# Kernel optimization log

Hardware: AMD Instinct MI355X
Metric: run time of the kernel (lower is better)

## Reference

```python
import jax, jax.numpy as jnp
import numpy as np

NINP = 1024
NHID = 1024
STEPS = 8
INITRANGE = 0.04
T, B = 256, 64

# DARTS_V1 recurrent genotype: (activation, predecessor-state index)
GENOTYPE = [("sigmoid", 0), ("relu", 1), ("relu", 1), ("identity", 1),
            ("tanh", 2), ("sigmoid", 5), ("tanh", 3), ("relu", 5)]

ACT = {
    "tanh": jnp.tanh,
    "relu": jax.nn.relu,
    "sigmoid": jax.nn.sigmoid,
    "identity": lambda x: x,
    "selu": jax.nn.selu,
}


def setup_inputs() -> dict:
    key = jax.random.key(0)
    k_in, k_w0, k_ws = jax.random.split(key, 3)
    inputs = jax.random.normal(k_in, (T, B, NINP), dtype=jnp.float32)
    hidden = jnp.zeros((1, B, NHID), dtype=jnp.float32)
    W0 = jax.random.uniform(k_w0, (NINP + NHID, 2 * NHID),
                            minval=-INITRANGE, maxval=INITRANGE, dtype=jnp.float32)
    Ws = jax.random.uniform(k_ws, (STEPS, NHID, 2 * NHID),
                            minval=-INITRANGE, maxval=INITRANGE, dtype=jnp.float32)
    return {"inputs": inputs, "hidden": hidden, "W0": W0, "Ws": Ws}


def _cell(x, h_prev, W0, Ws):
    # init state: highway combine of gated candidate with previous hidden
    xh = jnp.concatenate([x, h_prev], axis=-1)            # [B, ninp+nhid]
    c0, h0 = jnp.split(xh @ W0, 2, axis=-1)               # [B, nhid] each
    s0 = h_prev + jax.nn.sigmoid(c0) * (jnp.tanh(h0) - h_prev)
    states = [s0]
    for i, (name, pred) in enumerate(GENOTYPE):
        s_prev = states[pred]
        c, h = jnp.split(s_prev @ Ws[i], 2, axis=-1)      # [B, nhid] each
        s = s_prev + jax.nn.sigmoid(c) * (ACT[name](h) - s_prev)
        states.append(s)
    # output = mean over the DAG intermediate states (concat = range(1, steps+1))
    return jnp.mean(jnp.stack(states[1:], axis=0), axis=0)


def reference(inputs, hidden, W0, Ws):
    h0 = hidden[0]                                        # [B, nhid]

    def step(h, x_t):
        h_new = _cell(x_t, h, W0, Ws)
        return h_new, h_new

    _, hiddens = jax.lax.scan(step, h0, inputs)           # [T, B, nhid]
    return hiddens
```

## Files before the change

kernel.cpp:

```cpp
#include <hip/hip_runtime.h>
#include <math.h>


typedef __attribute__((ext_vector_type(8))) _Float16 half8;
typedef __attribute__((ext_vector_type(4))) float f32x4;
typedef __attribute__((ext_vector_type(4))) unsigned int u32x4;
typedef __attribute__((ext_vector_type(8))) unsigned short us8;

#define NH 1024
#define SCALE 2048.f
#define INVS  (1.f/2048.f)
#define WF_BYTES 83886080ull
#define FA_BYTES 1572864ull
#define T_STEPS  256

#define WBAR() asm volatile("s_barrier" ::: "memory")
#define LBAR() asm volatile("s_waitcnt lgkmcnt(0)\n\ts_barrier" ::: "memory")

__device__ __forceinline__ float sigf(float x){ return 1.f/(1.f+__expf(-x)); }
__device__ __forceinline__ void limbs2(float x, _Float16& a, _Float16& b){
    a = (_Float16)x; b = (_Float16)((x - (float)a)*SCALE);
}

struct Pre { const float* W0; const float* Ws; unsigned short* wf; };

__global__ __launch_bounds__(256) void preconv(Pre d) {
    int gid  = blockIdx.x * 4 + (threadIdx.x >> 6);
    int lane = threadIdx.x & 63;
    const float* W; unsigned short* dst; int nks, cg, ks;
    if (gid < 8192) {
        W = d.W0; dst = d.wf; nks = 64; cg = gid >> 6; ks = gid & 63;
    } else {
        int g = gid - 8192; int mm = g >> 12; int wi = g & 4095;
        W   = d.Ws + (size_t)mm * (1024 * 2048);
        dst = d.wf + 8388608ull + (size_t)mm * 4194304ull;
        nks = 32; cg = wi >> 5; ks = wi & 31;
    }
    int c  = cg * 16 + (lane & 15);
    int kb = ks * 32 + (lane >> 4) * 8;
    half8 h0, h1;
    #pragma unroll
    for (int j = 0; j < 8; ++j) {
        _Float16 p, q; limbs2(W[(size_t)(kb + j) * 2048 + c], p, q);
        h0[j] = p; h1[j] = q;
    }
    unsigned short* o = dst + ((size_t)cg * nks + ks) * 1024 + lane * 8;
    *(half8*)o         = h0;
    *(half8*)(o + 512) = h1;
}

__global__ __launch_bounds__(256) void initk(const float* hidden, char* fa, unsigned* flags) {
    int gid = blockIdx.x * 256 + threadIdx.x;
    if (gid < 1536) flags[gid] = (gid < 256) ? 1u : 0u;
    #pragma unroll
    for (int e = 0; e < 4; ++e) {
        int i = gid * 4 + e;
        int row = i >> 10, col = i & 1023;
        int rt = row >> 4, rowf = row & 15;
        int ksp = col >> 5, kin = col & 31;
        int lanep = (kin >> 3) * 16 + rowf;
        size_t off = (size_t)rt * 65536 + ((size_t)ksp * 64 + lanep) * 32 + (kin & 7) * 4;
        _Float16 u0, u1; limbs2(hidden[i], u0, u1);
        unsigned pk = (unsigned)__builtin_bit_cast(unsigned short, u0) |
                      ((unsigned)__builtin_bit_cast(unsigned short, u1) << 16);
        *(unsigned*)(fa + off) = pk;
    }
}

__device__ __forceinline__ void aload(const char* fa, int ks, int lane, half8& a0, half8& a1) {
    const char* p = fa + ((size_t)ks * 64 + lane) * 32;
    us8 q0 = *(const us8*)p;
    us8 q1 = *(const us8*)(p + 16);
    a0 = __builtin_bit_cast(half8, __builtin_shufflevector(q0, q1, 0,2,4,6,8,10,12,14));
    a1 = __builtin_bit_cast(half8, __builtin_shufflevector(q0, q1, 1,3,5,7,9,11,13,15));
}
__device__ __forceinline__ half8 ldw(const unsigned short* p) { return *(const half8*)p; }
__device__ __forceinline__ void mfma6(half8 a0, half8 a1, half8 w0, half8 w1,
                                      f32x4& x0, f32x4& x1) {
    x0 = __builtin_amdgcn_mfma_f32_16x16x32_f16(a0, w0, x0, 0, 0, 0);
    x1 = __builtin_amdgcn_mfma_f32_16x16x32_f16(a0, w1, x1, 0, 0, 0);
    x1 = __builtin_amdgcn_mfma_f32_16x16x32_f16(a1, w0, x1, 0, 0, 0);
}
__device__ __forceinline__ void rwrite1(float* arena, int wave, int lane,
        f32x4 c0, f32x4 c1, f32x4 h0, f32x4 h1) {
    float* b = arena + wave * 512;
    #pragma unroll
    for (int r = 0; r < 4; ++r) {
        b[lane * 4 + r]       = c0[r] + c1[r] * INVS;
        b[256 + lane * 4 + r] = h0[r] + h1[r] * INVS;
    }
}
__device__ __forceinline__ void rsum1(const float* arena, int idx, float& cs, float& hs) {
    float c = 0.f, h = 0.f;
    #pragma unroll
    for (int w = 0; w < 8; ++w) {
        c += arena[w * 512 + idx];
        h += arena[w * 512 + 256 + idx];
    }
    cs = c; hs = h;
}
__device__ __forceinline__ void fstore(char* fa, int offp, float v) {
    _Float16 u0, u1; limbs2(v, u0, u1);
    unsigned pk = (unsigned)__builtin_bit_cast(unsigned short, u0) |
                  ((unsigned)__builtin_bit_cast(unsigned short, u1) << 16);
    __hip_atomic_store((unsigned*)(fa + offp), pk, __ATOMIC_RELAXED, __HIP_MEMORY_SCOPE_AGENT);
}
template<int ACQ>
__device__ __forceinline__ void pollw(unsigned* f, unsigned tgt, int lane) {
    unsigned v = __hip_atomic_load(f + lane, __ATOMIC_RELAXED, __HIP_MEMORY_SCOPE_AGENT);
    while (__ballot(v < tgt)) {
        __builtin_amdgcn_s_sleep(2);
        v = __hip_atomic_load(f + lane, __ATOMIC_RELAXED, __HIP_MEMORY_SCOPE_AGENT);
    }
    if (ACQ)
        (void)__hip_atomic_load(f, __ATOMIC_ACQUIRE, __HIP_MEMORY_SCOPE_AGENT);
}
__device__ __forceinline__ void publish(unsigned* slot, unsigned v) {
    __hip_atomic_store(slot, v, __ATOMIC_RELAXED, __HIP_MEMORY_SCOPE_AGENT);
}

struct PK {
    const float* x; const float* hidden;
    const unsigned short* wf;
    char* fa; unsigned* flags; float* out;
};

__global__ __launch_bounds__(512, 2) void persist(PK p) {
    __shared__ unsigned short slab[65536];
    __shared__ float arena[4096];

    const int tid  = threadIdx.x;
    const int wave = tid >> 6, lane = tid & 63;
    const int l15 = lane & 15, lg = lane >> 4;
    const int lane8 = lane * 8, lg8 = lg * 8;
    const int bx = blockIdx.x;
    const int cg = (bx & 7) * 8 + ((bx >> 3) & 7);
    const int rt = bx >> 6;

    const unsigned short* wf0 = p.wf;
    const unsigned short* wfs[8];
    #pragma unroll
    for (int i = 0; i < 8; ++i) wfs[i] = p.wf + 8388608ull + (size_t)i * 4194304ull;

    char* FAH  = p.fa + (size_t)(0 * 4 + rt) * 65536;
    char* FAS0 = p.fa + (size_t)(1 * 4 + rt) * 65536;
    char* FAS1 = p.fa + (size_t)(2 * 4 + rt) * 65536;
    char* FAS2 = p.fa + (size_t)(3 * 4 + rt) * 65536;
    char* FAS3 = p.fa + (size_t)(4 * 4 + rt) * 65536;
    char* FAS5 = p.fa + (size_t)(5 * 4 + rt) * 65536;
    #define FLG(tn) (p.flags + ((tn) * 4 + rt) * 64)

    #define PFW(dst, wfp) do { \
        _Pragma("unroll") \
        for (int _i = 0; _i < 4; ++_i) { \
            const int _ks = wave * 4 + _i; \
            const unsigned short* _pc = (wfp) + ((size_t)cg * 32 + _ks) * 1024 + lane8; \
            const unsigned short* _ph = (wfp) + ((size_t)(cg + 64) * 32 + _ks) * 1024 + lane8; \
            dst[_i*4+0] = ldw(_pc); dst[_i*4+1] = ldw(_pc + 512); \
            dst[_i*4+2] = ldw(_ph); dst[_i*4+3] = ldw(_ph + 512); } } while (0)
    #define PFWX(dst) do { \
        _Pragma("unroll") \
        for (int _i = 0; _i < 4; ++_i) { \
            const int _ks = wave * 4 + _i; \
            const unsigned short* _pc = wf0 + ((size_t)cg * 64 + _ks) * 1024 + lane8; \
            const unsigned short* _ph = wf0 + ((size_t)(cg + 64) * 64 + _ks) * 1024 + lane8; \
            dst[_i*4+0] = ldw(_pc); dst[_i*4+1] = ldw(_pc + 512); \
            dst[_i*4+2] = ldw(_ph); dst[_i*4+3] = ldw(_ph + 512); } } while (0)
    #define ALD(dst0, dst1, fa) do { \
        _Pragma("unroll") \
        for (int _i = 0; _i < 4; ++_i) aload(fa, wave * 4 + _i, lane, dst0[_i], dst1[_i]); } while (0)
    #define MFM(w, a0v, a1v, X0, X1, Y0, Y1) do { \
        _Pragma("unroll") \
        for (int _i = 0; _i < 4; ++_i) { \
            mfma6(a0v[_i], a1v[_i], w[_i*4+0], w[_i*4+1], X0, X1); \
            mfma6(a0v[_i], a1v[_i], w[_i*4+2], w[_i*4+3], Y0, Y1); } } while (0)

    {
        const u32x4* sc = (const u32x4*)(wf0 + ((size_t)cg * 64 + 32) * 1024);
        const u32x4* sh = (const u32x4*)(wf0 + ((size_t)(cg + 64) * 64 + 32) * 1024);
        u32x4* dst = (u32x4*)slab;
        for (int i = tid; i < 4096; i += 512) { dst[i] = sc[i]; dst[4096 + i] = sh[i]; }
    }

    const int rowf = tid >> 4, colf = tid & 15;
    const size_t opos = (size_t)(rt * 16 + rowf) * NH + cg * 16 + colf;
    const int idx = colf * 4 + (rowf >> 2) * 64 + (rowf & 3);
    int offp;
    {
        int col = cg * 16 + colf;
        int ksp = col >> 5, kin = col & 31;
        int lanep = (kin >> 3) * 16 + rowf;
        offp = (ksp * 64 + lanep) * 32 + (kin & 7) * 4;
    }
    float hprev = 0.f, s0v = 0.f, s1v = 0.f, s2v = 0.f, s3v = 0.f, s5v = 0.f, runsum = 0.f;
    if (tid < 256) hprev = p.hidden[opos];
    const int xrow = rt * 16 + l15;
    __syncthreads();

    half8 wA[16], wB[16];
    PFW(wA, wfs[0]);
    PFWX(wB);

    for (int t = 0; t < T_STEPS; ++t) {
        const float* xt = p.x + (size_t)t * 65536;

        f32x4 c0 = {}, c1 = {}, h0 = {}, h1 = {};
        {
            half8 xa0[4], xa1[4];
            #pragma unroll
            for (int i = 0; i < 4; ++i) {
                const int ks = wave * 4 + i;
                const float* xp = xt + (size_t)xrow * NH + ks * 32 + lg8;
                float4 v0 = *(const float4*)xp, v1 = *(const float4*)(xp + 4);
                float fv[8] = {v0.x, v0.y, v0.z, v0.w, v1.x, v1.y, v1.z, v1.w};
                #pragma unroll
                for (int j = 0; j < 8; ++j) { _Float16 u, w2; limbs2(fv[j], u, w2); xa0[i][j] = u; xa1[i][j] = w2; }
            }
            if (wave == 7) {
                pollw<1>(FLG(0), t + 1, lane);
                asm volatile("s_waitcnt vmcnt(0)" ::: "memory");
            }
            MFM(wB, xa0, xa1, c0, c1, h0, h1);
        }
        WBAR();
        {
            half8 ha0[4], ha1[4];
            ALD(ha0, ha1, FAH);
            #pragma unroll
            for (int i = 0; i < 4; ++i) {
                const int kc = wave * 4 + i;
                const unsigned short* pc = &slab[kc * 1024 + lane8];
                const unsigned short* ph = &slab[(kc + 32) * 1024 + lane8];
                mfma6(ha0[i], ha1[i], *(const half8*)pc, *(const half8*)(pc + 512), c0, c1);
                mfma6(ha0[i], ha1[i], *(const half8*)ph, *(const half8*)(ph + 512), h0, h1);
            }
            rwrite1(arena, wave, lane, c0, c1, h0, h1);
        }
        LBAR();
        if (tid < 256) {
            float cs, hs; rsum1(arena, idx, cs, hs);
            s0v = hprev + sigf(cs) * (tanhf(hs) - hprev);
            fstore(FAS0, offp, s0v);
        }
        __syncthreads();
        if (tid == 0) publish(FLG(1) + cg, t + 1);
        PFW(wB, wfs[1]);

        if (wave == 7) pollw<0>(FLG(1), t + 1, lane);
        WBAR();
        half8 a0[4], a1[4];
        {
            ALD(a0, a1, FAS0);
            f32x4 X0 = {}, X1 = {}, Y0 = {}, Y1 = {};
            MFM(wA, a0, a1, X0, X1, Y0, Y1);
            rwrite1(arena, wave, lane, X0, X1, Y0, Y1);
        }
        LBAR();
        if (tid < 256) {
            float cs, hs; rsum1(arena, idx, cs, hs);
            s1v = s0v + sigf(cs) * (sigf(hs) - s0v);
            fstore(FAS1, offp, s1v);
            runsum = s1v;
        }
        __syncthreads();
        if (tid == 0) publish(FLG(2) + cg, t + 1);
        PFW(wA, wfs[2]);

        if (wave == 7) pollw<0>(FLG(2), t + 1, lane);
        WBAR();
        ALD(a0, a1, FAS1);
        {
            f32x4 X0 = {}, X1 = {}, Y0 = {}, Y1 = {};
            MFM(wB, a0, a1, X0, X1, Y0, Y1);
            rwrite1(arena, wave, lane, X0, X1, Y0, Y1);
        }
        LBAR();
        if (tid < 256) {
            float cs, hs; rsum1(arena, idx, cs, hs);
            s2v = s1v + sigf(cs) * (fmaxf(hs, 0.f) - s1v);
            fstore(FAS2, offp, s2v);
        }
        __syncthreads();
        if (tid == 0) publish(FLG(3) + cg, t + 1);
        PFW(wB, wfs[3]);
        {
            f32x4 X0 = {}, X1 = {}, Y0 = {}, Y1 = {};
            MFM(wA, a0, a1, X0, X1, Y0, Y1);
            rwrite1(arena, wave, lane, X0, X1, Y0, Y1);
        }
        LBAR();
        if (tid < 256) {
            float cs, hs; rsum1(arena, idx, cs, hs);
            s3v = s1v + sigf(cs) * (fmaxf(hs, 0.f) - s1v);
            fstore(FAS3, offp, s3v);
        }
        __syncthreads();
        if (tid == 0) publish(FLG(4) + cg, t + 1);
        PFW(wA, wfs[4]);
        {
            f32x4 X0 = {}, X1 = {}, Y0 = {}, Y1 = {};
            MFM(wB, a0, a1, X0, X1, Y0, Y1);
            rwrite1(arena, wave, lane, X0, X1, Y0, Y1);
        }
        LBAR();
        if (tid < 256) {
            float cs, hs; rsum1(arena, idx, cs, hs);
            float s4v = s1v + sigf(cs) * (hs - s1v);
            runsum += s2v + s3v + s4v;
        }
        WBAR();
        PFW(wB, wfs[6]);

        if (wave == 7) { pollw<0>(FLG(3), t + 1, lane); pollw<0>(FLG(4), t + 1, lane); }
        WBAR();
        {
            half8 b0[4], b1[4];
            ALD(a0, a1, FAS2);
            ALD(b0, b1, FAS3);
            f32x4 X0 = {}, X1 = {}, Y0 = {}, Y1 = {};
            MFM(wA, a0, a1, X0, X1, Y0, Y1);
            f32x4 U0 = {}, U1 = {}, V0 = {}, V1 = {};
            MFM(wB, b0, b1, U0, U1, V0, V1);
            rwrite1(arena, wave, lane, X0, X1, Y0, Y1);
            LBAR();
            if (tid < 256) {
                float cs, hs; rsum1(arena, idx, cs, hs);
                s5v = s2v + sigf(cs) * (tanhf(hs) - s2v);
                fstore(FAS5, offp, s5v);
            }
            __syncthreads();
            if (tid == 0) publish(FLG(5) + cg, t + 1);
            PFW(wA, wfs[5]);
            rwrite1(arena, wave, lane, U0, U1, V0, V1);
            LBAR();
            if (tid < 256) {
                float cs, hs; rsum1(arena, idx, cs, hs);
                float s7v = s3v + sigf(cs) * (tanhf(hs) - s3v);
                runsum += s5v + s7v;
            }
            WBAR();
            PFW(wB, wfs[7]);
        }

        if (wave == 7) pollw<0>(FLG(5), t + 1, lane);
        WBAR();
        {
            ALD(a0, a1, FAS5);
            f32x4 X0 = {}, X1 = {}, Y0 = {}, Y1 = {};
            MFM(wA, a0, a1, X0, X1, Y0, Y1);
            f32x4 U0 = {}, U1 = {}, V0 = {}, V1 = {};
            MFM(wB, a0, a1, U0, U1, V0, V1);
            rwrite1(arena, wave, lane, X0, X1, Y0, Y1);
            LBAR();
            float c6 = 0.f, h6 = 0.f;
            if (tid < 256) rsum1(arena, idx, c6, h6);
            LBAR();
            PFW(wA, wfs[0]);
            rwrite1(arena, wave, lane, U0, U1, V0, V1);
            LBAR();
            if (tid < 256) {
                float c8, h8; rsum1(arena, idx, c8, h8);
                float s6 = s5v + sigf(c6) * (sigf(h6) - s5v);
                float s8 = s5v + sigf(c8) * (fmaxf(h8, 0.f) - s5v);
                float v = 0.125f * (runsum + s6 + s8);
                p.out[(size_t)t * 65536 + opos] = v;
                fstore(FAH, offp, v);
                hprev = v;
            }
            __syncthreads();
            if (tid == 0) publish(FLG(0) + cg, t + 2);
            PFWX(wB);
        }
    }
    #undef FLG
    #undef PFW
    #undef PFWX
    #undef ALD
    #undef MFM
}

extern "C" void kernel_launch(void* const* d_in, const int* in_sizes, int n_in,
                              void* d_out, int out_size, void* d_ws, size_t ws_size,
                              hipStream_t stream) {
    (void)in_sizes; (void)n_in; (void)out_size; (void)ws_size;
    const float* inputs = (const float*)d_in[0];
    const float* hidden = (const float*)d_in[1];
    const float* W0     = (const float*)d_in[2];
    const float* Ws     = (const float*)d_in[3];
    float* out = (float*)d_out;

    char* base = (char*)d_ws;
    unsigned short* wf = (unsigned short*)base;
    char* fa = base + WF_BYTES;
    unsigned* flags = (unsigned*)(fa + FA_BYTES);

    initk<<<64, 256, 0, stream>>>(hidden, fa, flags);
    preconv<<<10240, 256, 0, stream>>>(Pre{W0, Ws, wf});

    PK pk{inputs, hidden, wf, fa, flags, out};
    void* args[] = {&pk};
    if (hipLaunchCooperativeKernel((void*)persist, dim3(256), dim3(512), args, 0, stream) != hipSuccess)
        persist<<<256, 512, 0, stream>>>(pk);
}
```

Baseline: 9.756 ms.

## Stream weights via global_load_lds into a double-buffered LDS ring

Replaces the register-held weight prefetch (two 16-entry half8 buffers) and the static LDS slab holding the hidden part of W0 with a two-slot LDS ring. Each slot is filled by direct global-to-LDS loads, and the next weight block is issued right after the current one is consumed. The aim is to free VGPRs and let the load engine overlap weight fetches with MFMA work. In exchange, prefetch depth drops to one half-matrix ahead. The recurrent W0 slice is now re-streamed from global memory every step. Correctness relies on the barriers draining the async LDS loads, since only lgkmcnt waits are added explicitly.

```diff
diff --git a/kernel.cpp b/kernel.cpp
--- a/kernel.cpp
+++ b/kernel.cpp
@@ -4,7 +4,6 @@
 
 typedef __attribute__((ext_vector_type(8))) _Float16 half8;
 typedef __attribute__((ext_vector_type(4))) float f32x4;
-typedef __attribute__((ext_vector_type(4))) unsigned int u32x4;
 typedef __attribute__((ext_vector_type(8))) unsigned short us8;
 
 #define NH 1024
@@ -14,8 +13,11 @@
 #define FA_BYTES 1572864ull
 #define T_STEPS  256
 
-#define WBAR() asm volatile("s_barrier" ::: "memory")
-#define LBAR() asm volatile("s_waitcnt lgkmcnt(0)\n\ts_barrier" ::: "memory")
+#define LGKM0() asm volatile("s_waitcnt lgkmcnt(0)" ::: "memory")
+#define LBAR()  asm volatile("s_waitcnt lgkmcnt(0)\n\ts_barrier" ::: "memory")
+
+typedef const __attribute__((address_space(1))) void* gas_ptr;
+typedef __attribute__((address_space(3))) void* las_ptr;
 
 __device__ __forceinline__ float sigf(float x){ return 1.f/(1.f+__expf(-x)); }
 __device__ __forceinline__ void limbs2(float x, _Float16& a, _Float16& b){
@@ -74,7 +76,6 @@
     a0 = __builtin_bit_cast(half8, __builtin_shufflevector(q0, q1, 0,2,4,6,8,10,12,14));
     a1 = __builtin_bit_cast(half8, __builtin_shufflevector(q0, q1, 1,3,5,7,9,11,13,15));
 }
-__device__ __forceinline__ half8 ldw(const unsigned short* p) { return *(const half8*)p; }
 __device__ __forceinline__ void mfma6(half8 a0, half8 a1, half8 w0, half8 w1,
                                       f32x4& x0, f32x4& x1) {
     x0 = __builtin_amdgcn_mfma_f32_16x16x32_f16(a0, w0, x0, 0, 0, 0);
@@ -126,21 +127,32 @@
 };
 
 __global__ __launch_bounds__(512, 2) void persist(PK p) {
-    __shared__ unsigned short slab[65536];
+    __shared__ char ring[2][65536];
     __shared__ float arena[4096];
 
-    const int tid  = threadIdx.x;
+    const int tid = threadIdx.x;
     const int wave = tid >> 6, lane = tid & 63;
     const int l15 = lane & 15, lg = lane >> 4;
-    const int lane8 = lane * 8, lg8 = lg * 8;
+    const int lg8 = lg * 8;
     const int bx = blockIdx.x;
     const int cg = (bx & 7) * 8 + ((bx >> 3) & 7);
     const int rt = bx >> 6;
 
     const unsigned short* wf0 = p.wf;
-    const unsigned short* wfs[8];
-    #pragma unroll
-    for (int i = 0; i < 8; ++i) wfs[i] = p.wf + 8388608ull + (size_t)i * 4194304ull;
+    const unsigned short* gB[20];
+    {
+        gB[0] = wf0 + (size_t)(cg * 64) * 1024;
+        gB[1] = wf0 + (size_t)((cg + 64) * 64) * 1024;
+        gB[2] = wf0 + (size_t)(cg * 64 + 32) * 1024;
+        gB[3] = wf0 + (size_t)((cg + 64) * 64 + 32) * 1024;
+        const int mo[8] = {0, 1, 2, 3, 4, 6, 5, 7};
+        #pragma unroll
+        for (int u = 0; u < 8; ++u) {
+            const unsigned short* wm = p.wf + 8388608ull + (size_t)mo[u] * 4194304ull;
+            gB[4 + 2 * u]     = wm + (size_t)cg * 32768;
+            gB[4 + 2 * u + 1] = wm + (size_t)(cg + 64) * 32768;
+        }
+    }
 
     char* FAH  = p.fa + (size_t)(0 * 4 + rt) * 65536;
     char* FAS0 = p.fa + (size_t)(1 * 4 + rt) * 65536;
@@ -150,37 +162,27 @@
     char* FAS5 = p.fa + (size_t)(5 * 4 + rt) * 65536;
     #define FLG(tn) (p.flags + ((tn) * 4 + rt) * 64)
 
-    #define PFW(dst, wfp) do { \
+    #define DMA(b) do { \
+        const char* _g = (const char*)gB[b] + wave * 8192 + lane * 16; \
+        char* _l = &ring[(b) & 1][wave * 8192]; \
+        _Pragma("unroll") \
+        for (int _i = 0; _i < 8; ++_i) \
+            __builtin_amdgcn_global_load_lds((gas_ptr)(_g + _i * 1024), \
+                                             (las_ptr)(_l + _i * 1024), 16, 0, 0); \
+    } while (0)
+    #define CONS(b, A0, A1, X0, X1) do { \
         _Pragma("unroll") \
         for (int _i = 0; _i < 4; ++_i) { \
-            const int _ks = wave * 4 + _i; \
-            const unsigned short* _pc = (wfp) + ((size_t)cg * 32 + _ks) * 1024 + lane8; \
-            const unsigned short* _ph = (wfp) + ((size_t)(cg + 64) * 32 + _ks) * 1024 + lane8; \
-            dst[_i*4+0] = ldw(_pc); dst[_i*4+1] = ldw(_pc + 512); \
-            dst[_i*4+2] = ldw(_ph); dst[_i*4+3] = ldw(_ph + 512); } } while (0)
-    #define PFWX(dst) do { \
-        _Pragma("unroll") \
-        for (int _i = 0; _i < 4; ++_i) { \
-            const int _ks = wave * 4 + _i; \
-            const unsigned short* _pc = wf0 + ((size_t)cg * 64 + _ks) * 1024 + lane8; \
-            const unsigned short* _ph = wf0 + ((size_t)(cg + 64) * 64 + _ks) * 1024 + lane8; \
-            dst[_i*4+0] = ldw(_pc); dst[_i*4+1] = ldw(_pc + 512); \
-            dst[_i*4+2] = ldw(_ph); dst[_i*4+3] = ldw(_ph + 512); } } while (0)
+            const char* _p = &ring[(b) & 1][(wave * 4 + _i) * 2048 + lane * 16]; \
+            half8 _w0 = *(const half8*)_p; \
+            half8 _w1 = *(const half8*)(_p + 1024); \
+            mfma6(A0[_i], A1[_i], _w0, _w1, X0, X1); \
+        } \
+    } while (0)
     #define ALD(dst0, dst1, fa) do { \
         _Pragma("unroll") \
-        for (int _i = 0; _i < 4; ++_i) aload(fa, wave * 4 + _i, lane, dst0[_i], dst1[_i]); } while (0)
-    #define MFM(w, a0v, a1v, X0, X1, Y0, Y1) do { \
-        _Pragma("unroll") \
-        for (int _i = 0; _i < 4; ++_i) { \
-            mfma6(a0v[_i], a1v[_i], w[_i*4+0], w[_i*4+1], X0, X1); \
-            mfma6(a0v[_i], a1v[_i], w[_i*4+2], w[_i*4+3], Y0, Y1); } } while (0)
-
-    {
-        const u32x4* sc = (const u32x4*)(wf0 + ((size_t)cg * 64 + 32) * 1024);
-        const u32x4* sh = (const u32x4*)(wf0 + ((size_t)(cg + 64) * 64 + 32) * 1024);
-        u32x4* dst = (u32x4*)slab;
-        for (int i = tid; i < 4096; i += 512) { dst[i] = sc[i]; dst[4096 + i] = sh[i]; }
-    }
+        for (int _i = 0; _i < 4; ++_i) aload(fa, wave * 4 + _i, lane, dst0[_i], dst1[_i]); \
+    } while (0)
 
     const int rowf = tid >> 4, colf = tid & 15;
     const size_t opos = (size_t)(rt * 16 + rowf) * NH + cg * 16 + colf;
@@ -195,14 +197,13 @@
     float hprev = 0.f, s0v = 0.f, s1v = 0.f, s2v = 0.f, s3v = 0.f, s5v = 0.f, runsum = 0.f;
     if (tid < 256) hprev = p.hidden[opos];
     const int xrow = rt * 16 + l15;
+
+    DMA(0); DMA(1);
     __syncthreads();
-
-    half8 wA[16], wB[16];
-    PFW(wA, wfs[0]);
-    PFWX(wB);
 
     for (int t = 0; t < T_STEPS; ++t) {
         const float* xt = p.x + (size_t)t * 65536;
+        half8 a0[4], a1[4];
 
         f32x4 c0 = {}, c1 = {}, h0 = {}, h1 = {};
         {
@@ -216,24 +217,16 @@
                 #pragma unroll
                 for (int j = 0; j < 8; ++j) { _Float16 u, w2; limbs2(fv[j], u, w2); xa0[i][j] = u; xa1[i][j] = w2; }
             }
-            if (wave == 7) {
-                pollw<1>(FLG(0), t + 1, lane);
-                asm volatile("s_waitcnt vmcnt(0)" ::: "memory");
-            }
-            MFM(wB, xa0, xa1, c0, c1, h0, h1);
-        }
-        WBAR();
+            CONS(0, xa0, xa1, c0, c1); LGKM0(); DMA(2);
+            CONS(1, xa0, xa1, h0, h1); LGKM0(); DMA(3);
+        }
+        if (wave == 7) pollw<1>(FLG(0), t + 1, lane);
+        __syncthreads();
         {
             half8 ha0[4], ha1[4];
             ALD(ha0, ha1, FAH);
-            #pragma unroll
-            for (int i = 0; i < 4; ++i) {
-                const int kc = wave * 4 + i;
-                const unsigned short* pc = &slab[kc * 1024 + lane8];
-                const unsigned short* ph = &slab[(kc + 32) * 1024 + lane8];
-                mfma6(ha0[i], ha1[i], *(const half8*)pc, *(const half8*)(pc + 512), c0, c1);
-                mfma6(ha0[i], ha1[i], *(const half8*)ph, *(const half8*)(ph + 512), h0, h1);
-            }
+            CONS(2, ha0, ha1, c0, c1); LGKM0(); DMA(4);
+            CONS(3, ha0, ha1, h0, h1); LGKM0(); DMA(5);
             rwrite1(arena, wave, lane, c0, c1, h0, h1);
         }
         LBAR();
@@ -244,15 +237,14 @@
         }
         __syncthreads();
         if (tid == 0) publish(FLG(1) + cg, t + 1);
-        PFW(wB, wfs[1]);
 
         if (wave == 7) pollw<0>(FLG(1), t + 1, lane);
-        WBAR();
-        half8 a0[4], a1[4];
-        {
-            ALD(a0, a1, FAS0);
-            f32x4 X0 = {}, X1 = {}, Y0 = {}, Y1 = {};
-            MFM(wA, a0, a1, X0, X1, Y0, Y1);
+        __syncthreads();
+        ALD(a0, a1, FAS0);
+        {
+            f32x4 X0 = {}, X1 = {}, Y0 = {}, Y1 = {};
+            CONS(4, a0, a1, X0, X1); LGKM0(); DMA(6);
+            CONS(5, a0, a1, Y0, Y1); LGKM0(); DMA(7);
             rwrite1(arena, wave, lane, X0, X1, Y0, Y1);
         }
         LBAR();
@@ -264,14 +256,14 @@
         }
         __syncthreads();
         if (tid == 0) publish(FLG(2) + cg, t + 1);
-        PFW(wA, wfs[2]);
 
         if (wave == 7) pollw<0>(FLG(2), t + 1, lane);
-        WBAR();
+        __syncthreads();
         ALD(a0, a1, FAS1);
         {
             f32x4 X0 = {}, X1 = {}, Y0 = {}, Y1 = {};
-            MFM(wB, a0, a1, X0, X1, Y0, Y1);
+            CONS(6, a0, a1, X0, X1); LGKM0(); DMA(8);
+            CONS(7, a0, a1, Y0, Y1); LGKM0(); DMA(9);
             rwrite1(arena, wave, lane, X0, X1, Y0, Y1);
         }
         LBAR();
@@ -282,10 +274,10 @@
         }
         __syncthreads();
         if (tid == 0) publish(FLG(3) + cg, t + 1);
-        PFW(wB, wfs[3]);
-        {
-            f32x4 X0 = {}, X1 = {}, Y0 = {}, Y1 = {};
-            MFM(wA, a0, a1, X0, X1, Y0, Y1);
+        {
+            f32x4 X0 = {}, X1 = {}, Y0 = {}, Y1 = {};
+            CONS(8, a0, a1, X0, X1); LGKM0(); DMA(10);
+            CONS(9, a0, a1, Y0, Y1); LGKM0(); DMA(11);
             rwrite1(arena, wave, lane, X0, X1, Y0, Y1);
         }
         LBAR();
@@ -296,10 +288,10 @@
         }
         __syncthreads();
         if (tid == 0) publish(FLG(4) + cg, t + 1);
-        PFW(wA, wfs[4]);
-        {
-            f32x4 X0 = {}, X1 = {}, Y0 = {}, Y1 = {};
-            MFM(wB, a0, a1, X0, X1, Y0, Y1);
+        {
+            f32x4 X0 = {}, X1 = {}, Y0 = {}, Y1 = {};
+            CONS(10, a0, a1, X0, X1); LGKM0(); DMA(12);
+            CONS(11, a0, a1, Y0, Y1); LGKM0(); DMA(13);
             rwrite1(arena, wave, lane, X0, X1, Y0, Y1);
         }
         LBAR();
@@ -308,19 +300,16 @@
             float s4v = s1v + sigf(cs) * (hs - s1v);
             runsum += s2v + s3v + s4v;
         }
-        WBAR();
-        PFW(wB, wfs[6]);
 
         if (wave == 7) { pollw<0>(FLG(3), t + 1, lane); pollw<0>(FLG(4), t + 1, lane); }
-        WBAR();
-        {
-            half8 b0[4], b1[4];
+        __syncthreads();
+        {
+            half8 bb0[4], bb1[4];
             ALD(a0, a1, FAS2);
-            ALD(b0, b1, FAS3);
-            f32x4 X0 = {}, X1 = {}, Y0 = {}, Y1 = {};
-            MFM(wA, a0, a1, X0, X1, Y0, Y1);
-            f32x4 U0 = {}, U1 = {}, V0 = {}, V1 = {};
-            MFM(wB, b0, b1, U0, U1, V0, V1);
+            ALD(bb0, bb1, FAS3);
+            f32x4 X0 = {}, X1 = {}, Y0 = {}, Y1 = {};
+            CONS(12, a0, a1, X0, X1); LGKM0(); DMA(14);
+            CONS(13, a0, a1, Y0, Y1); LGKM0(); DMA(15);
             rwrite1(arena, wave, lane, X0, X1, Y0, Y1);
             LBAR();
             if (tid < 256) {
@@ -330,7 +319,9 @@
             }
             __syncthreads();
             if (tid == 0) publish(FLG(5) + cg, t + 1);
-            PFW(wA, wfs[5]);
+            f32x4 U0 = {}, U1 = {}, V0 = {}, V1 = {};
+            CONS(14, bb0, bb1, U0, U1); LGKM0(); DMA(16);
+            CONS(15, bb0, bb1, V0, V1); LGKM0(); DMA(17);
             rwrite1(arena, wave, lane, U0, U1, V0, V1);
             LBAR();
             if (tid < 256) {
@@ -338,24 +329,23 @@
                 float s7v = s3v + sigf(cs) * (tanhf(hs) - s3v);
                 runsum += s5v + s7v;
             }
-            WBAR();
-            PFW(wB, wfs[7]);
         }
 
         if (wave == 7) pollw<0>(FLG(5), t + 1, lane);
-        WBAR();
+        __syncthreads();
         {
             ALD(a0, a1, FAS5);
             f32x4 X0 = {}, X1 = {}, Y0 = {}, Y1 = {};
-            MFM(wA, a0, a1, X0, X1, Y0, Y1);
-            f32x4 U0 = {}, U1 = {}, V0 = {}, V1 = {};
-            MFM(wB, a0, a1, U0, U1, V0, V1);
-            rwrite1(arena, wave, lane, X0, X1, Y0, Y1);
-            LBAR();
+            CONS(16, a0, a1, X0, X1); LGKM0(); DMA(18);
+            CONS(17, a0, a1, Y0, Y1); LGKM0(); DMA(19);
+            rwrite1(arena, wave, lane, X0, X1, Y0, Y1);
+            __syncthreads();
             float c6 = 0.f, h6 = 0.f;
             if (tid < 256) rsum1(arena, idx, c6, h6);
             LBAR();
-            PFW(wA, wfs[0]);
+            f32x4 U0 = {}, U1 = {}, V0 = {}, V1 = {};
+            CONS(18, a0, a1, U0, U1); LGKM0(); DMA(0);
+            CONS(19, a0, a1, V0, V1); LGKM0(); DMA(1);
             rwrite1(arena, wave, lane, U0, U1, V0, V1);
             LBAR();
             if (tid < 256) {
@@ -369,14 +359,12 @@
             }
             __syncthreads();
             if (tid == 0) publish(FLG(0) + cg, t + 2);
-            PFWX(wB);
         }
     }
     #undef FLG
-    #undef PFW
-    #undef PFWX
+    #undef DMA
+    #undef CONS
     #undef ALD
-    #undef MFM
 }
 
 extern "C" void kernel_launch(void* const* d_in, const int* in_sizes, int n_in,
```

Measured after the change: 26.34 ms. +170.0%, slower.
